# Optimization experiments

Hardware: AMD Instinct MI355X
Metric: run time of the kernel (lower is better)

The kernel has to match this reference:

```python
import jax, jax.numpy as jnp
import numpy as np

TOP_K = 2

def setup_inputs() -> dict:
    key = jax.random.key(0)
    ks = jax.random.split(key, 5)
    B, S, H, F, E = 4, 512, 1024, 3584, 8
    x = jax.random.normal(ks[0], (B, S, H), dtype=jnp.float32)
    gate_w = jax.random.normal(ks[1], (H, E), dtype=jnp.float32) * (1.0 / np.sqrt(H))
    w1 = jax.random.normal(ks[2], (E, F, H), dtype=jnp.float32) * (1.0 / np.sqrt(H))
    w3 = jax.random.normal(ks[3], (E, F, H), dtype=jnp.float32) * (1.0 / np.sqrt(H))
    w2 = jax.random.normal(ks[4], (E, H, F), dtype=jnp.float32) * (1.0 / np.sqrt(F))
    return {"x": x, "gate_w": gate_w, "w1": w1, "w3": w3, "w2": w2}


def reference(x, gate_w, w1, w3, w2):
    # MoE top-2 routing (Mixtral-style), dense-dispatch formulation.
    B, S, H = x.shape
    E = gate_w.shape[1]
    xt = x.reshape(-1, H)                      # [T, H] flattened tokens
    T = xt.shape[0]
    logits = xt @ gate_w                       # [T, E] gate logits
    top_w, top_i = jax.lax.top_k(logits, TOP_K)    # [T, K]
    top_w = jax.nn.softmax(top_w, axis=-1)         # softmax over selected-k logits
    # combine[t, e] = routing weight of expert e for token t (0 if not selected)
    combine = jnp.zeros((T, E), dtype=xt.dtype)
    combine = combine.at[jnp.arange(T)[:, None], top_i].add(top_w)
    # SwiGLU experts: y_e = w2_e @ (silu(w1_e x) * (w3_e x))
    h = jnp.einsum('th,efh->tef', xt, w1)      # [T, E, F]
    g = jnp.einsum('th,efh->tef', xt, w3)      # [T, E, F]
    act = jax.nn.silu(h) * g                   # [T, E, F]
    out_e = jnp.einsum('tef,ehf->teh', act, w2)  # [T, E, H]
    out = jnp.einsum('teh,te->th', out_e, combine)  # weighted combine over experts
    return out.reshape(B, S, H)
```

## Files before the change

### kernel.cpp

```cpp
#include <hip/hip_runtime.h>
#include <hip/hip_bf16.h>
#include <stdint.h>

#define TOKENS 2048
#define HDIM 1024
#define FDIM 3584
#define NEXP 8
#define BK 32

typedef __attribute__((ext_vector_type(8))) short short8;
typedef __attribute__((ext_vector_type(4))) float floatx4;

#define AS1 __attribute__((address_space(1)))
#define AS3 __attribute__((address_space(3)))

__device__ __forceinline__ void glds16(const void* g, void* l) {
  __builtin_amdgcn_global_load_lds((const AS1 void*)g, (AS3 void*)l, 16, 0, 0);
}

__device__ __forceinline__ unsigned short f2bf(float f) {
  union { float f; unsigned int u; } c; c.f = f;
  unsigned int u = c.u;
  u += 0x7fffu + ((u >> 16) & 1u);
  return (unsigned short)(u >> 16);
}

__device__ __forceinline__ unsigned int pk2bf(float a, float b) {
  __hip_bfloat162 h = __float22bfloat162_rn(make_float2(a, b));
  union { __hip_bfloat162 h; unsigned int u; } c; c.h = h;
  return c.u;
}

__global__ void gate_kernel(const float* __restrict__ x,
                            const float* __restrict__ gw,
                            int* __restrict__ top_e,
                            float* __restrict__ top_w) {
  int wv = threadIdx.x >> 6;
  int lane = threadIdx.x & 63;
  int t = blockIdx.x * 4 + wv;
  if (t >= TOKENS) return;
  float p[NEXP];
#pragma unroll
  for (int e = 0; e < NEXP; e++) p[e] = 0.f;
  const float* xr = x + (size_t)t * HDIM;
  for (int h = lane; h < HDIM; h += 64) {
    float xv = xr[h];
    const float4* g4 = (const float4*)(gw + (size_t)h * NEXP);
    float4 a = g4[0], b = g4[1];
    p[0] += xv * a.x; p[1] += xv * a.y; p[2] += xv * a.z; p[3] += xv * a.w;
    p[4] += xv * b.x; p[5] += xv * b.y; p[6] += xv * b.z; p[7] += xv * b.w;
  }
#pragma unroll
  for (int e = 0; e < NEXP; e++) {
#pragma unroll
    for (int off = 32; off > 0; off >>= 1) p[e] += __shfl_xor(p[e], off, 64);
  }
  if (lane == 0) {
    int i0 = 0;
    for (int e = 1; e < NEXP; e++) if (p[e] > p[i0]) i0 = e;
    int i1 = (i0 == 0) ? 1 : 0;
    for (int e = 0; e < NEXP; e++) if (e != i0 && p[e] > p[i1]) i1 = e;
    float l0 = p[i0], l1 = p[i1];
    float e1 = __expf(l1 - l0);
    float s = 1.f + e1;
    top_e[t * 2] = i0; top_e[t * 2 + 1] = i1;
    top_w[t * 2] = 1.f / s; top_w[t * 2 + 1] = e1 / s;
  }
}

__global__ void route_kernel(const int* __restrict__ top_e,
                             int* __restrict__ count,
                             int* __restrict__ offs,
                             int* __restrict__ tok_of,
                             int* __restrict__ slot_of) {
  __shared__ int hist[NEXP];
  __shared__ int cur[NEXP];
  int tid = threadIdx.x;
  if (tid < NEXP) hist[tid] = 0;
  __syncthreads();
  int e[4];
#pragma unroll
  for (int j = 0; j < 4; j++) {
    int i = tid * 4 + j;
    e[j] = top_e[i];
    atomicAdd(&hist[e[j]], 1);
  }
  __syncthreads();
  if (tid == 0) {
    int o = 0;
    for (int k = 0; k < NEXP; k++) {
      offs[k] = o; cur[k] = o; count[k] = hist[k]; o += hist[k];
    }
  }
  __syncthreads();
#pragma unroll
  for (int j = 0; j < 4; j++) {
    int i = tid * 4 + j;
    int g = atomicAdd(&cur[e[j]], 1);
    tok_of[g] = i >> 1;
    slot_of[i] = g;
  }
}

__global__ void xconv_kernel(const float* __restrict__ x,
                             unsigned short* __restrict__ xbf) {
  int i = (blockIdx.x * blockDim.x + threadIdx.x) * 4;
  float4 v = *(const float4*)(x + i);
  uint2 pk;
  pk.x = pk2bf(v.x, v.y);
  pk.y = pk2bf(v.z, v.w);
  *(uint2*)(xbf + i) = pk;
}

#define WCONV_N (29360128ull)
#define WCONV_BLK 3584
__global__ void wconv_kernel(const float* __restrict__ w1,
                             const float* __restrict__ w3,
                             const float* __restrict__ w2,
                             unsigned short* __restrict__ b1,
                             unsigned short* __restrict__ b3,
                             unsigned short* __restrict__ b2) {
  int z = blockIdx.y;
  const float* src = (z == 0) ? w1 : (z == 1) ? w3 : w2;
  unsigned short* dst = (z == 0) ? b1 : (z == 1) ? b3 : b2;
  int t4 = threadIdx.x * 4;
  for (size_t base = (size_t)blockIdx.x * 2048; base < WCONV_N;
       base += (size_t)WCONV_BLK * 2048) {
    float4 a = *(const float4*)(src + base + t4);
    float4 b = *(const float4*)(src + base + 1024 + t4);
    uint2 pa, pb;
    pa.x = pk2bf(a.x, a.y); pa.y = pk2bf(a.z, a.w);
    pb.x = pk2bf(b.x, b.y); pb.y = pk2bf(b.z, b.w);
    *(uint2*)(dst + base + t4) = pa;
    *(uint2*)(dst + base + 1024 + t4) = pb;
  }
}

#define G1_BM 128
#define G1_BF 64

__global__ __launch_bounds__(256, 3)
void gemm1_kernel(const unsigned short* __restrict__ xbf,
                  const unsigned short* __restrict__ w1b,
                  const unsigned short* __restrict__ w3b,
                  const int* __restrict__ count,
                  const int* __restrict__ offs,
                  const int* __restrict__ tok_of,
                  unsigned short* __restrict__ act) {
  int e = blockIdx.z;
  int cnt = count[e];
  int m0 = blockIdx.y * G1_BM;
  if (m0 >= cnt) return;
  int f0 = blockIdx.x * G1_BF;
  int off_e = offs[e];

  __shared__ __align__(16) unsigned short sA[2 * G1_BM * 32];
  __shared__ __align__(16) unsigned short sB1[2 * G1_BF * 32];
  __shared__ __align__(16) unsigned short sB3[2 * G1_BF * 32];

  int tid = threadIdx.x;
  int lane = tid & 63, wv = tid >> 6;

  const unsigned short* ag[2];
  char* alb[2];
#pragma unroll
  for (int p = 0; p < 2; p++) {
    int c = tid + p * 256;
    int row = c >> 2, slot = c & 3;
    int gch = slot ^ ((row >> 1) & 3);
    int r = m0 + row;
    int tok = tok_of[off_e + (r < cnt ? r : 0)];
    ag[p] = xbf + (size_t)tok * HDIM + gch * 8;
    alb[p] = (char*)sA + (wv * 64 + p * 256) * 16;
  }
  const unsigned short *b1g, *b3g;
  char *b1l, *b3l;
  {
    int row = tid >> 2, slot = tid & 3;
    int gch = slot ^ ((row >> 1) & 3);
    size_t wrow = (size_t)e * FDIM + f0 + row;
    b1g = w1b + wrow * HDIM + gch * 8;
    b3g = w3b + wrow * HDIM + gch * 8;
    b1l = (char*)sB1 + (wv * 64) * 16;
    b3l = (char*)sB3 + (wv * 64) * 16;
  }

  int lrow = lane & 15, quad = lane >> 4;
  int wm = wv >> 1, wn = wv & 1;

  floatx4 acc1[4][2], acc3[4][2];
#pragma unroll
  for (int i = 0; i < 4; i++)
#pragma unroll
    for (int j = 0; j < 2; j++) {
      acc1[i][j] = (floatx4){0.f, 0.f, 0.f, 0.f};
      acc3[i][j] = (floatx4){0.f, 0.f, 0.f, 0.f};
    }

  const int NT = HDIM / BK;

#pragma unroll
  for (int p = 0; p < 2; p++) glds16(ag[p], alb[p]);
  glds16(b1g, b1l);
  glds16(b3g, b3l);
  __syncthreads();

  int cur = 0;
  for (int t = 0; t < NT; t++) {
    if (t + 1 < NT) {
      int k = (t + 1) * BK;
      int nb = cur ^ 1;
#pragma unroll
      for (int p = 0; p < 2; p++) glds16(ag[p] + k, alb[p] + nb * 8192);
      glds16(b1g + k, b1l + nb * 4096);
      glds16(b3g + k, b3l + nb * 4096);
    }

    const unsigned short* sAc = sA + cur * (G1_BM * 32);
    const unsigned short* sB1c = sB1 + cur * (G1_BF * 32);
    const unsigned short* sB3c = sB3 + cur * (G1_BF * 32);

    short8 af[4], b1f[2], b3f[2];
#pragma unroll
    for (int ms = 0; ms < 4; ms++) {
      int r = wm * 64 + ms * 16 + lrow;
      int sl = quad ^ ((r >> 1) & 3);
      af[ms] = *(const short8*)(sAc + r * 32 + sl * 8);
    }
#pragma unroll
    for (int ns = 0; ns < 2; ns++) {
      int r = wn * 32 + ns * 16 + lrow;
      int sl = quad ^ ((r >> 1) & 3);
      b1f[ns] = *(const short8*)(sB1c + r * 32 + sl * 8);
      b3f[ns] = *(const short8*)(sB3c + r * 32 + sl * 8);
    }
#pragma unroll
    for (int ms = 0; ms < 4; ms++)
#pragma unroll
      for (int ns = 0; ns < 2; ns++) {
        acc1[ms][ns] = __builtin_amdgcn_mfma_f32_16x16x32_bf16(af[ms], b1f[ns], acc1[ms][ns], 0, 0, 0);
        acc3[ms][ns] = __builtin_amdgcn_mfma_f32_16x16x32_bf16(af[ms], b3f[ns], acc3[ms][ns], 0, 0, 0);
      }

    __syncthreads();
    cur ^= 1;
  }

#pragma unroll
  for (int ms = 0; ms < 4; ms++) {
#pragma unroll
    for (int reg = 0; reg < 4; reg++) {
      int slot = m0 + wm * 64 + ms * 16 + quad * 4 + reg;
      if (slot < cnt) {
        unsigned short* ar = act + (size_t)(off_e + slot) * FDIM + f0 + wn * 32;
#pragma unroll
        for (int ns = 0; ns < 2; ns++) {
          float h = acc1[ms][ns][reg];
          float g = acc3[ms][ns][reg];
          float a = h / (1.f + __expf(-h)) * g;
          ar[ns * 16 + lrow] = f2bf(a);
        }
      }
    }
  }
}

#define G2_BM 128
#define G2_BN 128
#define SPLITK 2
#define G2_KS (FDIM / SPLITK)

__global__ __launch_bounds__(256, 3)
void gemm2_kernel(const unsigned short* __restrict__ act,
                  const unsigned short* __restrict__ w2b,
                  const int* __restrict__ count,
                  const int* __restrict__ offs,
                  float* __restrict__ part) {
  int zz = blockIdx.z;
  int e = zz & 7, sk = zz >> 3;
  int cnt = count[e];
  int m0 = blockIdx.y * G2_BM;
  if (m0 >= cnt) return;
  int h0 = blockIdx.x * G2_BN;
  int off_e = offs[e];
  int kb = sk * G2_KS;

  __shared__ __align__(16) unsigned short sA[2 * G2_BM * 32];
  __shared__ __align__(16) unsigned short sB[2 * G2_BN * 32];

  int tid = threadIdx.x;
  int lane = tid & 63, wv = tid >> 6;

  const unsigned short* ag[2];
  char* alb[2];
#pragma unroll
  for (int p = 0; p < 2; p++) {
    int c = tid + p * 256;
    int row = c >> 2, slot = c & 3;
    int gch = slot ^ ((row >> 1) & 3);
    int r = m0 + row;
    int rr = (r < cnt ? r : 0);
    ag[p] = act + (size_t)(off_e + rr) * FDIM + kb + gch * 8;
    alb[p] = (char*)sA + (wv * 64 + p * 256) * 16;
  }
  const unsigned short* bg[2];
  char* blb[2];
#pragma unroll
  for (int p = 0; p < 2; p++) {
    int c = tid + p * 256;
    int row = c >> 2, slot = c & 3;
    int gch = slot ^ ((row >> 1) & 3);
    bg[p] = w2b + ((size_t)e * HDIM + h0 + row) * FDIM + kb + gch * 8;
    blb[p] = (char*)sB + (wv * 64 + p * 256) * 16;
  }

  int lrow = lane & 15, quad = lane >> 4;
  int wm = wv >> 1, wn = wv & 1;

  floatx4 acc[4][4];
#pragma unroll
  for (int i = 0; i < 4; i++)
#pragma unroll
    for (int j = 0; j < 4; j++) acc[i][j] = (floatx4){0.f, 0.f, 0.f, 0.f};

  const int NT = G2_KS / BK;

#pragma unroll
  for (int p = 0; p < 2; p++) { glds16(ag[p], alb[p]); glds16(bg[p], blb[p]); }
  __syncthreads();

  int cur = 0;
  for (int t = 0; t < NT; t++) {
    if (t + 1 < NT) {
      int k = (t + 1) * BK;
      int nb = cur ^ 1;
#pragma unroll
      for (int p = 0; p < 2; p++) {
        glds16(ag[p] + k, alb[p] + nb * 8192);
        glds16(bg[p] + k, blb[p] + nb * 8192);
      }
    }

    const unsigned short* sAc = sA + cur * (G2_BM * 32);
    const unsigned short* sBc = sB + cur * (G2_BN * 32);

    short8 af[4], bf[4];
#pragma unroll
    for (int ms = 0; ms < 4; ms++) {
      int r = wm * 64 + ms * 16 + lrow;
      int sl = quad ^ ((r >> 1) & 3);
      af[ms] = *(const short8*)(sAc + r * 32 + sl * 8);
    }
#pragma unroll
    for (int ns = 0; ns < 4; ns++) {
      int r = wn * 64 + ns * 16 + lrow;
      int sl = quad ^ ((r >> 1) & 3);
      bf[ns] = *(const short8*)(sBc + r * 32 + sl * 8);
    }
#pragma unroll
    for (int ms = 0; ms < 4; ms++)
#pragma unroll
      for (int ns = 0; ns < 4; ns++)
        acc[ms][ns] = __builtin_amdgcn_mfma_f32_16x16x32_bf16(af[ms], bf[ns], acc[ms][ns], 0, 0, 0);

    __syncthreads();
    cur ^= 1;
  }

#pragma unroll
  for (int ms = 0; ms < 4; ms++) {
#pragma unroll
    for (int reg = 0; reg < 4; reg++) {
      int slot = m0 + wm * 64 + ms * 16 + quad * 4 + reg;
      if (slot < cnt) {
        float* crow = part + ((size_t)sk * 4096 + off_e + slot) * HDIM + h0 + wn * 64;
#pragma unroll
        for (int ns = 0; ns < 4; ns++)
          crow[ns * 16 + lrow] = acc[ms][ns][reg];
      }
    }
  }
}

__global__ void combine_kernel(const float* __restrict__ part,
                               const int* __restrict__ slot_of,
                               const float* __restrict__ top_w,
                               float* __restrict__ out) {
  int t = blockIdx.x;
  int g0 = slot_of[t * 2], g1 = slot_of[t * 2 + 1];
  float w0 = top_w[t * 2], w1 = top_w[t * 2 + 1];
  int i = threadIdx.x;
  float4 s0 = {0.f, 0.f, 0.f, 0.f}, s1 = {0.f, 0.f, 0.f, 0.f};
#pragma unroll
  for (int sk = 0; sk < SPLITK; sk++) {
    float4 a = ((const float4*)(part + ((size_t)sk * 4096 + g0) * HDIM))[i];
    float4 b = ((const float4*)(part + ((size_t)sk * 4096 + g1) * HDIM))[i];
    s0.x += a.x; s0.y += a.y; s0.z += a.z; s0.w += a.w;
    s1.x += b.x; s1.y += b.y; s1.z += b.z; s1.w += b.w;
  }
  float4 r;
  r.x = w0 * s0.x + w1 * s1.x;
  r.y = w0 * s0.y + w1 * s1.y;
  r.z = w0 * s0.z + w1 * s1.z;
  r.w = w0 * s0.w + w1 * s1.w;
  ((float4*)(out + (size_t)t * HDIM))[i] = r;
}

extern "C" void kernel_launch(void* const* d_in, const int* in_sizes, int n_in,
                              void* d_out, int out_size, void* d_ws, size_t ws_size,
                              hipStream_t stream) {
  const float* x  = (const float*)d_in[0];
  const float* gw = (const float*)d_in[1];
  const float* w1 = (const float*)d_in[2];
  const float* w3 = (const float*)d_in[3];
  const float* w2 = (const float*)d_in[4];
  float* out = (float*)d_out;

  char* ws = (char*)d_ws;
  const size_t MB = 1ull << 20;
  float* top_w = (float*)(ws);
  int* top_e   = (int*)(ws + 16384);
  int* slot_of = (int*)(ws + 32768);
  int* tok_of  = (int*)(ws + 49152);
  int* count   = (int*)(ws + 65536);
  int* offs    = (int*)(ws + 65536 + 64);

  unsigned short* xbf = (unsigned short*)(ws + 1 * MB);
  unsigned short* act = (unsigned short*)(ws + 5 * MB);
  unsigned short* w2b = (unsigned short*)(ws + 35 * MB);
  unsigned short* w1b = (unsigned short*)(ws + 94 * MB);
  unsigned short* w3b = (unsigned short*)(ws + 150 * MB);
  float* part = (float*)(ws + 94 * MB);

  gate_kernel<<<TOKENS / 4, 256, 0, stream>>>(x, gw, top_e, top_w);
  route_kernel<<<1, 1024, 0, stream>>>(top_e, count, offs, tok_of, slot_of);
  xconv_kernel<<<(TOKENS * HDIM) / (256 * 4), 256, 0, stream>>>(x, xbf);
  wconv_kernel<<<dim3(WCONV_BLK, 3), 256, 0, stream>>>(w1, w3, w2, w1b, w3b, w2b);
  gemm1_kernel<<<dim3(FDIM / G1_BF, TOKENS / G1_BM, NEXP), 256, 0, stream>>>(
      xbf, w1b, w3b, count, offs, tok_of, act);
  gemm2_kernel<<<dim3(HDIM / G2_BN, TOKENS / G2_BM, NEXP * SPLITK), 256, 0, stream>>>(
      act, w2b, count, offs, part);
  combine_kernel<<<TOKENS, 256, 0, stream>>>(part, slot_of, top_w, out);
}
```

Baseline: 534.7 us.

## Fuse fp32-to-bf16 weight conversion into expert GEMM tile loads

Removes the separate weight conversion kernel that turned w1, w3 and w2 into bf16 copies in the workspace. Both GEMMs now read fp32 weights straight from global memory into registers, pack them to bf16, and write them into the double-buffered LDS tile after the MFMA block. This drops a full extra read-and-write pass over the weights. In exchange, weight tiles are fetched as fp32, so each GEMM reads twice the bytes per tile, and weights re-read by several M-blocks cost more. Staging through registers also replaces the async direct-to-LDS loads for the B operand.

```diff
diff --git a/kernel.cpp b/kernel.cpp
--- a/kernel.cpp
+++ b/kernel.cpp
@@ -29,6 +29,13 @@
   __hip_bfloat162 h = __float22bfloat162_rn(make_float2(a, b));
   union { __hip_bfloat162 h; unsigned int u; } c; c.h = h;
   return c.u;
+}
+
+__device__ __forceinline__ short8 pack_bf16(float4 c0, float4 c1) {
+  union { short8 s; uint4 u; } o;
+  o.u.x = pk2bf(c0.x, c0.y); o.u.y = pk2bf(c0.z, c0.w);
+  o.u.z = pk2bf(c1.x, c1.y); o.u.w = pk2bf(c1.z, c1.w);
+  return o.s;
 }
 
 __global__ void gate_kernel(const float* __restrict__ x,
@@ -112,37 +119,13 @@
   *(uint2*)(xbf + i) = pk;
 }
 
-#define WCONV_N (29360128ull)
-#define WCONV_BLK 3584
-__global__ void wconv_kernel(const float* __restrict__ w1,
-                             const float* __restrict__ w3,
-                             const float* __restrict__ w2,
-                             unsigned short* __restrict__ b1,
-                             unsigned short* __restrict__ b3,
-                             unsigned short* __restrict__ b2) {
-  int z = blockIdx.y;
-  const float* src = (z == 0) ? w1 : (z == 1) ? w3 : w2;
-  unsigned short* dst = (z == 0) ? b1 : (z == 1) ? b3 : b2;
-  int t4 = threadIdx.x * 4;
-  for (size_t base = (size_t)blockIdx.x * 2048; base < WCONV_N;
-       base += (size_t)WCONV_BLK * 2048) {
-    float4 a = *(const float4*)(src + base + t4);
-    float4 b = *(const float4*)(src + base + 1024 + t4);
-    uint2 pa, pb;
-    pa.x = pk2bf(a.x, a.y); pa.y = pk2bf(a.z, a.w);
-    pb.x = pk2bf(b.x, b.y); pb.y = pk2bf(b.z, b.w);
-    *(uint2*)(dst + base + t4) = pa;
-    *(uint2*)(dst + base + 1024 + t4) = pb;
-  }
-}
-
 #define G1_BM 128
 #define G1_BF 64
 
 __global__ __launch_bounds__(256, 3)
 void gemm1_kernel(const unsigned short* __restrict__ xbf,
-                  const unsigned short* __restrict__ w1b,
-                  const unsigned short* __restrict__ w3b,
+                  const float* __restrict__ w1,
+                  const float* __restrict__ w3,
                   const int* __restrict__ count,
                   const int* __restrict__ offs,
                   const int* __restrict__ tok_of,
@@ -173,16 +156,16 @@
     ag[p] = xbf + (size_t)tok * HDIM + gch * 8;
     alb[p] = (char*)sA + (wv * 64 + p * 256) * 16;
   }
-  const unsigned short *b1g, *b3g;
-  char *b1l, *b3l;
+  const float *b1g, *b3g;
+  unsigned short *b1l, *b3l;
   {
     int row = tid >> 2, slot = tid & 3;
     int gch = slot ^ ((row >> 1) & 3);
     size_t wrow = (size_t)e * FDIM + f0 + row;
-    b1g = w1b + wrow * HDIM + gch * 8;
-    b3g = w3b + wrow * HDIM + gch * 8;
-    b1l = (char*)sB1 + (wv * 64) * 16;
-    b3l = (char*)sB3 + (wv * 64) * 16;
+    b1g = w1 + wrow * HDIM + gch * 8;
+    b3g = w3 + wrow * HDIM + gch * 8;
+    b1l = sB1 + tid * 8;
+    b3l = sB3 + tid * 8;
   }
 
   int lrow = lane & 15, quad = lane >> 4;
@@ -201,19 +184,28 @@
 
 #pragma unroll
   for (int p = 0; p < 2; p++) glds16(ag[p], alb[p]);
-  glds16(b1g, b1l);
-  glds16(b3g, b3l);
+  {
+    float4 u0 = *(const float4*)(b1g);
+    float4 u1 = *(const float4*)(b1g + 4);
+    float4 v0 = *(const float4*)(b3g);
+    float4 v1 = *(const float4*)(b3g + 4);
+    *(short8*)b1l = pack_bf16(u0, u1);
+    *(short8*)b3l = pack_bf16(v0, v1);
+  }
   __syncthreads();
 
   int cur = 0;
   for (int t = 0; t < NT; t++) {
+    int nb = cur ^ 1;
+    float4 u0, u1, v0, v1;
     if (t + 1 < NT) {
       int k = (t + 1) * BK;
-      int nb = cur ^ 1;
 #pragma unroll
       for (int p = 0; p < 2; p++) glds16(ag[p] + k, alb[p] + nb * 8192);
-      glds16(b1g + k, b1l + nb * 4096);
-      glds16(b3g + k, b3l + nb * 4096);
+      u0 = *(const float4*)(b1g + k);
+      u1 = *(const float4*)(b1g + k + 4);
+      v0 = *(const float4*)(b3g + k);
+      v1 = *(const float4*)(b3g + k + 4);
     }
 
     const unsigned short* sAc = sA + cur * (G1_BM * 32);
@@ -242,8 +234,12 @@
         acc3[ms][ns] = __builtin_amdgcn_mfma_f32_16x16x32_bf16(af[ms], b3f[ns], acc3[ms][ns], 0, 0, 0);
       }
 
+    if (t + 1 < NT) {
+      *(short8*)(b1l + nb * (G1_BF * 32)) = pack_bf16(u0, u1);
+      *(short8*)(b3l + nb * (G1_BF * 32)) = pack_bf16(v0, v1);
+    }
     __syncthreads();
-    cur ^= 1;
+    cur = nb;
   }
 
 #pragma unroll
@@ -272,7 +268,7 @@
 
 __global__ __launch_bounds__(256, 3)
 void gemm2_kernel(const unsigned short* __restrict__ act,
-                  const unsigned short* __restrict__ w2b,
+                  const float* __restrict__ w2,
                   const int* __restrict__ count,
                   const int* __restrict__ offs,
                   float* __restrict__ part) {
@@ -303,15 +299,15 @@
     ag[p] = act + (size_t)(off_e + rr) * FDIM + kb + gch * 8;
     alb[p] = (char*)sA + (wv * 64 + p * 256) * 16;
   }
-  const unsigned short* bg[2];
-  char* blb[2];
+  const float* bg[2];
+  unsigned short* bl[2];
 #pragma unroll
   for (int p = 0; p < 2; p++) {
     int c = tid + p * 256;
     int row = c >> 2, slot = c & 3;
     int gch = slot ^ ((row >> 1) & 3);
-    bg[p] = w2b + ((size_t)e * HDIM + h0 + row) * FDIM + kb + gch * 8;
-    blb[p] = (char*)sB + (wv * 64 + p * 256) * 16;
+    bg[p] = w2 + ((size_t)e * HDIM + h0 + row) * FDIM + kb + gch * 8;
+    bl[p] = sB + c * 8;
   }
 
   int lrow = lane & 15, quad = lane >> 4;
@@ -326,18 +322,27 @@
   const int NT = G2_KS / BK;
 
 #pragma unroll
-  for (int p = 0; p < 2; p++) { glds16(ag[p], alb[p]); glds16(bg[p], blb[p]); }
+  for (int p = 0; p < 2; p++) glds16(ag[p], alb[p]);
+#pragma unroll
+  for (int p = 0; p < 2; p++) {
+    float4 u0 = *(const float4*)(bg[p]);
+    float4 u1 = *(const float4*)(bg[p] + 4);
+    *(short8*)(bl[p]) = pack_bf16(u0, u1);
+  }
   __syncthreads();
 
   int cur = 0;
   for (int t = 0; t < NT; t++) {
+    int nb = cur ^ 1;
+    float4 u0[2], u1[2];
     if (t + 1 < NT) {
       int k = (t + 1) * BK;
-      int nb = cur ^ 1;
+#pragma unroll
+      for (int p = 0; p < 2; p++) glds16(ag[p] + k, alb[p] + nb * 8192);
 #pragma unroll
       for (int p = 0; p < 2; p++) {
-        glds16(ag[p] + k, alb[p] + nb * 8192);
-        glds16(bg[p] + k, blb[p] + nb * 8192);
+        u0[p] = *(const float4*)(bg[p] + k);
+        u1[p] = *(const float4*)(bg[p] + k + 4);
       }
     }
 
@@ -363,8 +368,13 @@
       for (int ns = 0; ns < 4; ns++)
         acc[ms][ns] = __builtin_amdgcn_mfma_f32_16x16x32_bf16(af[ms], bf[ns], acc[ms][ns], 0, 0, 0);
 
+    if (t + 1 < NT) {
+#pragma unroll
+      for (int p = 0; p < 2; p++)
+        *(short8*)(bl[p] + nb * (G2_BN * 32)) = pack_bf16(u0[p], u1[p]);
+    }
     __syncthreads();
-    cur ^= 1;
+    cur = nb;
   }
 
 #pragma unroll
@@ -427,18 +437,14 @@
 
   unsigned short* xbf = (unsigned short*)(ws + 1 * MB);
   unsigned short* act = (unsigned short*)(ws + 5 * MB);
-  unsigned short* w2b = (unsigned short*)(ws + 35 * MB);
-  unsigned short* w1b = (unsigned short*)(ws + 94 * MB);
-  unsigned short* w3b = (unsigned short*)(ws + 150 * MB);
-  float* part = (float*)(ws + 94 * MB);
+  float* part = (float*)(ws + 35 * MB);
 
   gate_kernel<<<TOKENS / 4, 256, 0, stream>>>(x, gw, top_e, top_w);
   route_kernel<<<1, 1024, 0, stream>>>(top_e, count, offs, tok_of, slot_of);
   xconv_kernel<<<(TOKENS * HDIM) / (256 * 4), 256, 0, stream>>>(x, xbf);
-  wconv_kernel<<<dim3(WCONV_BLK, 3), 256, 0, stream>>>(w1, w3, w2, w1b, w3b, w2b);
   gemm1_kernel<<<dim3(FDIM / G1_BF, TOKENS / G1_BM, NEXP), 256, 0, stream>>>(
-      xbf, w1b, w3b, count, offs, tok_of, act);
+      xbf, w1, w3, count, offs, tok_of, act);
   gemm2_kernel<<<dim3(HDIM / G2_BN, TOKENS / G2_BM, NEXP * SPLITK), 256, 0, stream>>>(
-      act, w2b, count, offs, part);
+      act, w2, count, offs, part);
   combine_kernel<<<TOKENS, 256, 0, stream>>>(part, slot_of, top_w, out);
 }
```

Result: faster. 508.2 us (-5.0%).
